# Optimization experiments

Hardware: AMD Instinct MI355X
Metric: run time of the kernel (lower is better)

The kernel has to match this reference:

```python
import jax, jax.numpy as jnp
import numpy as np

HIDDEN = 4096
N_HEADS = 32
N_KV_HEADS = 8
HEAD_DIM = HIDDEN // N_HEADS  # 128
GROUPS = N_HEADS // N_KV_HEADS  # 4
ATTN_MULT = 0.08838834764831845  # 1/sqrt(head_dim)
MAX_ATTN_VAL = 30.0
NEG_INF = -1e30


def setup_inputs() -> dict:
    key = jax.random.key(0)
    ks = jax.random.split(key, 5)
    B, S = 2, 2048
    hidden_states = jax.random.normal(ks[0], (B, S, HIDDEN), dtype=jnp.float32)
    scale = 1.0 / np.sqrt(HIDDEN)
    Wq = jax.random.normal(ks[1], (HIDDEN, N_HEADS * HEAD_DIM), dtype=jnp.float32) * scale
    Wk = jax.random.normal(ks[2], (HIDDEN, N_KV_HEADS * HEAD_DIM), dtype=jnp.float32) * scale
    Wv = jax.random.normal(ks[3], (HIDDEN, N_KV_HEADS * HEAD_DIM), dtype=jnp.float32) * scale
    Wo = jax.random.normal(ks[4], (N_HEADS * HEAD_DIM, HIDDEN), dtype=jnp.float32) * scale
    return {"hidden_states": hidden_states, "Wq": Wq, "Wk": Wk, "Wv": Wv, "Wo": Wo}


def reference(hidden_states, Wq, Wk, Wv, Wo):
    B, S, _ = hidden_states.shape
    # projections
    q = (hidden_states @ Wq).reshape(B, S, N_HEADS, HEAD_DIM).transpose(0, 2, 1, 3)      # bhsd
    k = (hidden_states @ Wk).reshape(B, S, N_KV_HEADS, HEAD_DIM).transpose(0, 2, 1, 3)   # bksd
    v = (hidden_states @ Wv).reshape(B, S, N_KV_HEADS, HEAD_DIM).transpose(0, 2, 1, 3)
    # GQA: expand kv heads to query heads
    k = jnp.repeat(k, GROUPS, axis=1)  # [B, N_HEADS, S, D]
    v = jnp.repeat(v, GROUPS, axis=1)
    # scaled scores with Grok-style tanh soft-cap
    scores = jnp.einsum('bhqd,bhkd->bhqk', q, k) * ATTN_MULT
    scores = MAX_ATTN_VAL * jnp.tanh(scores / MAX_ATTN_VAL)
    # causal mask
    causal = jnp.tril(jnp.ones((S, S), dtype=bool))
    scores = jnp.where(causal[None, None], scores, NEG_INF)
    probs = jax.nn.softmax(scores.astype(jnp.float32), axis=-1).astype(v.dtype)
    out = jnp.einsum('bhqk,bhkd->bhqd', probs, v)          # [B, H, S, D]
    out = out.transpose(0, 2, 1, 3).reshape(B, S, N_HEADS * HEAD_DIM)
    return out @ Wo
```

## Files before the change

kernel.cpp:

```cpp
#include <hip/hip_runtime.h>
#include <hip/hip_bf16.h>
#include <type_traits>
#include <utility>
#include <cmath>

#define HIDDEN 4096
#define NHEADS 32
#define NKV 8
#define HD 128
#define BB 2
#define SS 2048
#define NTOK (BB*SS)
#define ATTN_MULT 0.08838834764831845f

using bf16x8 = __attribute__((ext_vector_type(8))) short;
using f32x4  = __attribute__((ext_vector_type(4))) float;

using gas = __attribute__((address_space(1))) const void;
using las = __attribute__((address_space(3))) void;

__device__ __forceinline__ unsigned short f2bf(float f){
  unsigned int u = __builtin_bit_cast(unsigned int, f);
  u += 0x7fffu + ((u >> 16) & 1u);
  return (unsigned short)(u >> 16);
}
__device__ __forceinline__ unsigned int cvtpk(float lo, float hi){
  unsigned int r;
  asm("v_cvt_pk_bf16_f32 %0, %1, %2" : "=v"(r) : "v"(lo), "v"(hi));
  return r;
}
__device__ __forceinline__ float exp2_hw(float x){
  float r;
  asm("v_exp_f32 %0, %1" : "=v"(r) : "v"(x));
  return r;
}

#define LOG2E 1.4426950408889634f
#define C1L  (-5.3433149e-4f)
#define C2L  (2.3748069e-7f)
#define B30L (-43.280851227f)

__global__ void cvt_f32_bf16_k(const float* __restrict__ in, unsigned short* __restrict__ out, int n8){
  int i = blockIdx.x * blockDim.x + threadIdx.x;
  if (i >= n8) return;
  const float4* p = (const float4*)in + (size_t)i * 2;
  float4 a = p[0], b = p[1];
  bf16x8 o;
  o[0]=f2bf(a.x); o[1]=f2bf(a.y); o[2]=f2bf(a.z); o[3]=f2bf(a.w);
  o[4]=f2bf(b.x); o[5]=f2bf(b.y); o[6]=f2bf(b.z); o[7]=f2bf(b.w);
  ((bf16x8*)out)[i] = o;
}

__global__ void transpose_cvt_k(const float* __restrict__ W, unsigned short* __restrict__ WT, int K, int N){
  __shared__ float tile[32][33];
  int n0 = blockIdx.x * 32, k0 = blockIdx.y * 32;
  int tx = threadIdx.x, ty = threadIdx.y;
  #pragma unroll
  for (int i = 0; i < 4; ++i)
    tile[ty*4+i][tx] = W[(size_t)(k0 + ty*4 + i) * N + n0 + tx];
  __syncthreads();
  #pragma unroll
  for (int i = 0; i < 4; ++i)
    WT[(size_t)(n0 + ty*4 + i) * K + k0 + tx] = f2bf(tile[tx][ty*4+i]);
}

__global__ void transpose_v_k(const unsigned short* __restrict__ in, unsigned short* __restrict__ out){
  __shared__ unsigned short tile[32][33];
  int c0 = blockIdx.x * 32, r0 = blockIdx.y * 32;
  int tx = threadIdx.x, ty = threadIdx.y;
  #pragma unroll
  for (int i = 0; i < 4; ++i)
    tile[ty*4+i][tx] = in[(size_t)(r0 + ty*4 + i) * 2048 + 1024 + c0 + tx];
  __syncthreads();
  #pragma unroll
  for (int i = 0; i < 4; ++i){
    int c = c0 + ty*4 + i, r = r0 + tx;
    out[((size_t)((r >> 11) * 1024 + c)) * 2048 + (r & 2047)] = tile[tx][ty*4+i];
  }
}

template<typename OutT>
__global__ __launch_bounds__(256, 3)
void gemm_bt_k(const unsigned short* __restrict__ A,
               const unsigned short* __restrict__ BT,
               OutT* __restrict__ C, int M, int N, int K){
  __shared__ __align__(16) unsigned short As[128*32];
  __shared__ __align__(16) unsigned short Bs[128*32];
  const int m0 = blockIdx.y * 128, n0 = blockIdx.x * 128;
  const int tid = threadIdx.x, w = tid >> 6, lane = tid & 63;
  const int wr = w >> 1, wc = w & 1;
  const int lrow = lane & 15, lk = (lane >> 4) * 8;
  const int arow = lane >> 2, acol = (lane & 3) * 8;

  f32x4 acc[4][4] = {};

  for (int k0 = 0; k0 < K; k0 += 32){
    #pragma unroll
    for (int i = 0; i < 2; ++i){
      int chunk = w*2 + i;
      const unsigned short* ga = A  + (size_t)(m0 + chunk*16 + arow) * K + k0 + acol;
      const unsigned short* gb = BT + (size_t)(n0 + chunk*16 + arow) * K + k0 + acol;
      __builtin_amdgcn_global_load_lds((gas*)ga, (las*)(As + chunk*512), 16, 0, 0);
      __builtin_amdgcn_global_load_lds((gas*)gb, (las*)(Bs + chunk*512), 16, 0, 0);
    }
    __syncthreads();
    bf16x8 af[4], bfr[4];
    #pragma unroll
    for (int m = 0; m < 4; ++m) af[m]  = *(const bf16x8*)&As[(wr*64 + m*16 + lrow)*32 + lk];
    #pragma unroll
    for (int n = 0; n < 4; ++n) bfr[n] = *(const bf16x8*)&Bs[(wc*64 + n*16 + lrow)*32 + lk];
    #pragma unroll
    for (int m = 0; m < 4; ++m)
      #pragma unroll
      for (int n = 0; n < 4; ++n)
        acc[m][n] = __builtin_amdgcn_mfma_f32_16x16x32_bf16(af[m], bfr[n], acc[m][n], 0, 0, 0);
    __syncthreads();
  }

  const int crow = (lane >> 4) * 4, ccol = lane & 15;
  #pragma unroll
  for (int m = 0; m < 4; ++m)
    #pragma unroll
    for (int n = 0; n < 4; ++n){
      size_t base = (size_t)(m0 + wr*64 + m*16 + crow) * N + n0 + wc*64 + n*16 + ccol;
      #pragma unroll
      for (int r = 0; r < 4; ++r){
        float v = acc[m][n][r];
        if constexpr (std::is_same<OutT, unsigned short>::value) C[base + (size_t)r*N] = f2bf(v);
        else                                                     C[base + (size_t)r*N] = v;
      }
    }
}

#define GBAR() asm volatile("s_barrier" ::: "memory")

#define GEMM_PHASE(P, VMN, STAGE_STMT)                                          \
  {                                                                             \
    bf16x8 af[2][2];                                                            \
    _Pragma("unroll") for (int mi = 0; mi < 2; ++mi)                            \
    _Pragma("unroll") for (int kk = 0; kk < 2; ++kk){                           \
      int row = wm*128 + (P)*32 + mi*16 + lrow;                                 \
      int c8 = (kk*4 + lhi) ^ (row & 7);                                        \
      af[mi][kk] = *(const bf16x8*)&As[cur][row*64 + c8*8];                     \
    }                                                                           \
    if ((P) == 0){                                                              \
      _Pragma("unroll") for (int nf = 0; nf < 4; ++nf)                          \
      _Pragma("unroll") for (int kk = 0; kk < 2; ++kk){                         \
        int row = wn*64 + nf*16 + lrow;                                         \
        int c8 = (kk*4 + lhi) ^ (row & 7);                                      \
        bf[nf][kk] = *(const bf16x8*)&Bs[cur][row*64 + c8*8];                   \
      }                                                                         \
    }                                                                           \
    STAGE_STMT;                                                                 \
    asm volatile("s_waitcnt vmcnt(" #VMN ")");                                  \
    GBAR();                                                                     \
    __builtin_amdgcn_s_setprio(1);                                              \
    _Pragma("unroll") for (int mi = 0; mi < 2; ++mi)                            \
    _Pragma("unroll") for (int nf = 0; nf < 4; ++nf)                            \
    _Pragma("unroll") for (int kk = 0; kk < 2; ++kk)                            \
      acc[(P)*2+mi][nf] = __builtin_amdgcn_mfma_f32_16x16x32_bf16(              \
          af[mi][kk], bf[nf][kk], acc[(P)*2+mi][nf], 0, 0, 0);                  \
    __builtin_amdgcn_s_setprio(0);                                              \
    GBAR();                                                                     \
  }

template<typename OutT>
__global__ __launch_bounds__(512, 2)
void gemm8_k(const unsigned short* __restrict__ A,
             const unsigned short* __restrict__ BT,
             OutT* __restrict__ C, int M, int N, int K, float scale){
  __shared__ __align__(16) unsigned short As[2][256*64];
  __shared__ __align__(16) unsigned short Bs[2][256*64];

  const int nbx = N >> 8;
  const int id = blockIdx.x + blockIdx.y * nbx;
  const int nwg = nbx * (M >> 8);
  const int swz = (id & 7) * (nwg >> 3) + (id >> 3);
  const int m0 = (swz / nbx) << 8, n0 = (swz % nbx) << 8;

  const int tid = threadIdx.x, w = tid >> 6, lane = tid & 63;
  const int wm = w >> 2, wn = w & 3;
  const int lrow = lane & 15, lhi = lane >> 4;
  const int l3 = lane >> 3, k8l = lane & 7;
  const int NT = K >> 6;

  f32x4 acc[8][4] = {};
  bf16x8 bf[4][2];

  auto stageB = [&](int t, int s, int half){
    #pragma unroll
    for (int j = 0; j < 2; ++j){
      int row0 = half*128 + j*64 + w*8;
      int row = row0 + l3;
      const unsigned short* g = BT + (size_t)(n0 + row) * K + t*64 + ((k8l ^ (row & 7)) << 3);
      __builtin_amdgcn_global_load_lds((gas*)g, (las*)(&Bs[s][0] + row0*64), 16, 0, 0);
    }
  };
  auto stageA = [&](int t, int s, int g2){
    #pragma unroll
    for (int j = 0; j < 2; ++j){
      int g = g2 + j;
      int row0 = ((w >= 4) ? 128 : 0) + g*32 + (w & 3)*8;
      int row = row0 + l3;
      const unsigned short* ga = A + (size_t)(m0 + row) * K + t*64 + ((k8l ^ (row & 7)) << 3);
      __builtin_amdgcn_global_load_lds((gas*)ga, (las*)(&As[s][0] + row0*64), 16, 0, 0);
    }
  };

  stageB(0, 0, 0); stageB(0, 0, 1); stageA(0, 0, 0); stageA(0, 0, 2);
  asm volatile("s_waitcnt vmcnt(3)");
  GBAR();

  for (int t = 0; t < NT - 1; ++t){
    const int cur = t & 1, nxt = cur ^ 1;
    GEMM_PHASE(0, 4, stageB(t+1, nxt, 0));
    GEMM_PHASE(1, 5, stageB(t+1, nxt, 1));
    GEMM_PHASE(2, 6, stageA(t+1, nxt, 0));
    GEMM_PHASE(3, 3, stageA(t+1, nxt, 2));
  }
  {
    const int cur = (NT - 1) & 1;
    GEMM_PHASE(0, 2, (void)0);
    GEMM_PHASE(1, 1, (void)0);
    GEMM_PHASE(2, 0, (void)0);
    GEMM_PHASE(3, 0, (void)0);
  }

  #pragma unroll
  for (int mf = 0; mf < 8; ++mf)
    #pragma unroll
    for (int nf = 0; nf < 4; ++nf){
      size_t base = (size_t)(m0 + wm*128 + mf*16 + lhi*4) * N + n0 + wn*64 + nf*16 + lrow;
      #pragma unroll
      for (int r = 0; r < 4; ++r){
        float v = acc[mf][nf][r] * scale;
        if constexpr (std::is_same<OutT, unsigned short>::value) C[base + (size_t)r*N] = f2bf(v);
        else                                                     C[base + (size_t)r*N] = v;
      }
    }
}

__global__ __launch_bounds__(512, 2)
void attn_k(const unsigned short* __restrict__ Q,
            const unsigned short* __restrict__ KVp,
            const unsigned short* __restrict__ VTp,
            unsigned short* __restrict__ ctx){
  __shared__ __align__(16) unsigned short Ks[2][64*128];
  __shared__ __align__(16) unsigned short Vt[2][128*64];
  __shared__ __align__(16) unsigned short Ps[8][1024];

  const int Wb = blockIdx.x;
  const int xcd = Wb & 7, sI = Wb >> 3;
  const int gsub = sI >> 5;
  const int inner = sI & 31;
  const int hsH = inner >> 3;
  const int fi = inner & 7;
  const int group = xcd*2 + gsub;
  const int b = group >> 3, kvh = group & 7;
  const int h = kvh*4 + hsH;

  const int tid = threadIdx.x, w = tid >> 6, lane = tid & 63;
  const int nt = 32 - 2*fi;
  const int lrow = lane & 15, lhi = lane >> 4;
  const int strip = (w < 4) ? fi : (15 - fi);
  const int qwb = strip*128 + (w & 3)*32;
  const int xorv = (lrow & 3) << 4;

  bf16x8 qf[2][4];
  {
    const unsigned short* qb = Q + (size_t)(b*SS + qwb + lrow) * 4096 + h*HD + lhi*8;
    #pragma unroll
    for (int qg = 0; qg < 2; ++qg)
      #pragma unroll
      for (int ks = 0; ks < 4; ++ks)
        qf[qg][ks] = *(const bf16x8*)(qb + (size_t)qg*16*4096 + ks*32);
  }

  f32x4 o[8][2] = {};
  float psum[2] = {0.f, 0.f};

  const unsigned short* Kbh  = KVp + (size_t)b * SS * 2048 + kvh * HD;
  const unsigned short* VTbh = VTp + ((size_t)b * 1024 + kvh * HD) * SS;

  auto STAGE = [&](int db, int t){
    #pragma unroll
    for (int it = 0; it < 2; ++it){
      int cbase = it*512 + w*64;
      int c = cbase + lane;
      int kkv = c >> 4, kc = c & 15;
      const unsigned short* gk = Kbh + (size_t)(t*64 + kkv) * 2048 + ((kc ^ (kkv & 7)) << 3);
      __builtin_amdgcn_global_load_lds((gas*)gk, (las*)(&Ks[db][0] + cbase*8), 16, 0, 0);
      int vd = c >> 3, vc = c & 7;
      const unsigned short* gv = VTbh + (size_t)vd * SS + t*64 + ((vc ^ ((vd ^ (vd >> 3)) & 7)) << 3);
      __builtin_amdgcn_global_load_lds((gas*)gv, (las*)(&Vt[db][0] + cbase*8), 16, 0, 0);
    }
  };

  STAGE(0, 0);
  __syncthreads();

  for (int t = 0; t < nt; ++t){
    const int db = t & 1;
    if (t + 1 < nt) STAGE(db ^ 1, t + 1);

    if (t*64 <= qwb + 31){
      const char* Kc = (const char*)&Ks[db][0];
      const char* Vc = (const char*)&Vt[db][0];
      char* Pw = (char*)&Ps[w][0];

      auto body = [&](auto DIAG){
        #pragma unroll
        for (int hh = 0; hh < 2; ++hh){
          f32x4 sacc[2][2];
          #pragma unroll
          for (int cc = 0; cc < 2; ++cc){
            const int row = (hh*2 + cc)*16 + lrow;
            bf16x8 kf[4];
            #pragma unroll
            for (int ks = 0; ks < 4; ++ks){
              int kbyte = (row*256 + (ks*32 + lhi*8)*2) ^ ((row & 7) << 4);
              kf[ks] = *(const bf16x8*)(Kc + kbyte);
            }
            f32x4 s0 = {0.f,0.f,0.f,0.f}, s1 = {0.f,0.f,0.f,0.f};
            __builtin_amdgcn_s_setprio(1);
            #pragma unroll
            for (int ks = 0; ks < 4; ++ks){
              s0 = __builtin_amdgcn_mfma_f32_16x16x32_bf16(kf[ks], qf[0][ks], s0, 0, 0, 0);
              s1 = __builtin_amdgcn_mfma_f32_16x16x32_bf16(kf[ks], qf[1][ks], s1, 0, 0, 0);
            }
            __builtin_amdgcn_s_setprio(0);
            sacc[0][cc] = s0; sacc[1][cc] = s1;
          }

          #pragma unroll
          for (int qg = 0; qg < 2; ++qg){
            const int qglob = qwb + qg*16 + lrow;
            #pragma unroll
            for (int cc = 0; cc < 2; ++cc){
              float pv[4];
              #pragma unroll
              for (int r = 0; r < 4; ++r){
                float s = __builtin_amdgcn_fmed3f(sacc[qg][cc][r], -25.f, 25.f);
                float s2 = s*s, s4 = s2*s2;
                float wv = __builtin_fmaf(s2, C1L, LOG2E);
                wv = __builtin_fmaf(s4, C2L, wv);
                float p = exp2_hw(__builtin_fmaf(s, wv, B30L));
                if constexpr (decltype(DIAG)::value){
                  int kvg = t*64 + (hh*2 + cc)*16 + lhi*4 + r;
                  p = (kvg <= qglob) ? p : 0.f;
                }
                psum[qg] += p;
                pv[r] = p;
              }
              uint2 pk;
              pk.x = cvtpk(pv[0], pv[1]);
              pk.y = cvtpk(pv[2], pv[3]);
              *(uint2*)(Pw + qg*1024 + lrow*64 + ((cc*32 + lhi*8) ^ xorv)) = pk;
            }
          }

          bf16x8 pf0 = *(const bf16x8*)(Pw +        lrow*64 + ((lhi*16) ^ xorv));
          bf16x8 pf1 = *(const bf16x8*)(Pw + 1024 + lrow*64 + ((lhi*16) ^ xorv));
          __builtin_amdgcn_s_setprio(1);
          #pragma unroll
          for (int df = 0; df < 8; ++df){
            int d = df*16 + lrow;
            int vbyte = (d*128 + (hh*32 + lhi*8)*2) ^ (((d ^ (d >> 3)) & 7) << 4);
            bf16x8 vf = *(const bf16x8*)(Vc + vbyte);
            o[df][0] = __builtin_amdgcn_mfma_f32_16x16x32_bf16(vf, pf0, o[df][0], 0, 0, 0);
            o[df][1] = __builtin_amdgcn_mfma_f32_16x16x32_bf16(vf, pf1, o[df][1], 0, 0, 0);
          }
          __builtin_amdgcn_s_setprio(0);
        }
      };
      if (t == (qwb >> 6)) body(std::true_type{});
      else                 body(std::false_type{});
    }
    __syncthreads();
  }

  #pragma unroll
  for (int qg = 0; qg < 2; ++qg){
    float sum = psum[qg];
    sum += __shfl_xor(sum, 16);
    sum += __shfl_xor(sum, 32);
    float inv = 1.f / sum;
    unsigned short* base = ctx + (size_t)(b*SS + qwb + qg*16 + lrow) * 4096 + h*HD + lhi*4;
    #pragma unroll
    for (int df = 0; df < 8; ++df){
      uint2 pk;
      pk.x = cvtpk(o[df][qg][0] * inv, o[df][qg][1] * inv);
      pk.y = cvtpk(o[df][qg][2] * inv, o[df][qg][3] * inv);
      *(uint2*)(base + df*16) = pk;
    }
  }
}

#define O_HSB   ((size_t)0)
#define O_WQT   ((size_t)33554432)
#define O_WKT   ((size_t)67108864)
#define O_WVT   ((size_t)75497472)
#define O_WOT   ((size_t)83886080)
#define O_Q     ((size_t)117440512)
#define O_KV    ((size_t)150994944)
#define O_CTX   ((size_t)167772160)
#define WS_NEED ((size_t)201326592)

extern "C" void kernel_launch(void* const* d_in, const int* in_sizes, int n_in,
                              void* d_out, int out_size, void* d_ws, size_t ws_size,
                              hipStream_t stream){
  if (ws_size < WS_NEED) return;
  const float* hs = (const float*)d_in[0];
  const float* Wq = (const float*)d_in[1];
  const float* Wk = (const float*)d_in[2];
  const float* Wv = (const float*)d_in[3];
  const float* Wo = (const float*)d_in[4];
  char* ws = (char*)d_ws;
  unsigned short* hsb = (unsigned short*)(ws + O_HSB);
  unsigned short* WqT = (unsigned short*)(ws + O_WQT);
  unsigned short* WkT = (unsigned short*)(ws + O_WKT);
  unsigned short* WvT = (unsigned short*)(ws + O_WVT);
  unsigned short* WoT = (unsigned short*)(ws + O_WOT);
  unsigned short* Qb  = (unsigned short*)(ws + O_Q);
  unsigned short* KVb = (unsigned short*)(ws + O_KV);
  unsigned short* ctxb= (unsigned short*)(ws + O_CTX);
  unsigned short* VTb = (unsigned short*)(ws + O_WQT);

  cvt_f32_bf16_k<<<dim3((NTOK*HIDDEN/8)/256), dim3(256), 0, stream>>>(hs, hsb, NTOK*HIDDEN/8);
  transpose_cvt_k<<<dim3(128,128), dim3(32,8), 0, stream>>>(Wq, WqT, 4096, 4096);
  transpose_cvt_k<<<dim3(32,128),  dim3(32,8), 0, stream>>>(Wk, WkT, 4096, 1024);
  transpose_cvt_k<<<dim3(32,128),  dim3(32,8), 0, stream>>>(Wv, WvT, 4096, 1024);
  transpose_cvt_k<<<dim3(128,128), dim3(32,8), 0, stream>>>(Wo, WoT, 4096, 4096);
  gemm8_k<unsigned short><<<dim3(16,16), dim3(512), 0, stream>>>(hsb, WqT, Qb, 4096, 4096, 4096, ATTN_MULT);
  gemm_bt_k<unsigned short><<<dim3(16,32), dim3(256), 0, stream>>>(hsb, WkT, KVb, 4096, 2048, 4096);
  transpose_v_k<<<dim3(32,128), dim3(32,8), 0, stream>>>(KVb, VTb);
  attn_k<<<dim3(512), dim3(512), 0, stream>>>(Qb, KVb, VTb, ctxb);
  gemm8_k<float><<<dim3(16,16), dim3(512), 0, stream>>>(ctxb, WoT, (float*)d_out, 4096, 4096, 4096, 1.0f);
}
```

Before: 553.9 us.

## Double query rows per wave in attention to reuse K/V fragments

Each wave in the attention kernel now handles 64 query rows (four 16-row groups) instead of 32. Every K and V fragment read from LDS therefore feeds twice as many MFMAs, and the grid halves to 256 blocks. The causal tile count and strip pairing are rescaled to match, and the per-wave P scratch buffer in shared memory is doubled. The cost is many more live registers (Q fragments, output accumulators and row sums), which risks spilling under the existing launch bounds, plus less parallelism across blocks.

```diff
diff --git a/kernel.cpp b/kernel.cpp
--- a/kernel.cpp
+++ b/kernel.cpp
@@ -247,37 +247,37 @@
             unsigned short* __restrict__ ctx){
   __shared__ __align__(16) unsigned short Ks[2][64*128];
   __shared__ __align__(16) unsigned short Vt[2][128*64];
-  __shared__ __align__(16) unsigned short Ps[8][1024];
+  __shared__ __align__(16) unsigned short Ps[8][2048];
 
   const int Wb = blockIdx.x;
   const int xcd = Wb & 7, sI = Wb >> 3;
-  const int gsub = sI >> 5;
-  const int inner = sI & 31;
-  const int hsH = inner >> 3;
-  const int fi = inner & 7;
+  const int gsub = sI >> 4;
+  const int inner = sI & 15;
+  const int hsH = inner >> 2;
+  const int fi = inner & 3;
   const int group = xcd*2 + gsub;
   const int b = group >> 3, kvh = group & 7;
   const int h = kvh*4 + hsH;
 
   const int tid = threadIdx.x, w = tid >> 6, lane = tid & 63;
-  const int nt = 32 - 2*fi;
+  const int nt = (8 - fi) * 4;
   const int lrow = lane & 15, lhi = lane >> 4;
-  const int strip = (w < 4) ? fi : (15 - fi);
-  const int qwb = strip*128 + (w & 3)*32;
+  const int strip = (w < 4) ? fi : (7 - fi);
+  const int qwb = strip*256 + (w & 3)*64;
   const int xorv = (lrow & 3) << 4;
 
-  bf16x8 qf[2][4];
+  bf16x8 qf[4][4];
   {
     const unsigned short* qb = Q + (size_t)(b*SS + qwb + lrow) * 4096 + h*HD + lhi*8;
     #pragma unroll
-    for (int qg = 0; qg < 2; ++qg)
+    for (int qg = 0; qg < 4; ++qg)
       #pragma unroll
       for (int ks = 0; ks < 4; ++ks)
         qf[qg][ks] = *(const bf16x8*)(qb + (size_t)qg*16*4096 + ks*32);
   }
 
-  f32x4 o[8][2] = {};
-  float psum[2] = {0.f, 0.f};
+  f32x4 o[8][4] = {};
+  float psum[4] = {0.f, 0.f, 0.f, 0.f};
 
   const unsigned short* Kbh  = KVp + (size_t)b * SS * 2048 + kvh * HD;
   const unsigned short* VTbh = VTp + ((size_t)b * 1024 + kvh * HD) * SS;
@@ -303,7 +303,7 @@
     const int db = t & 1;
     if (t + 1 < nt) STAGE(db ^ 1, t + 1);
 
-    if (t*64 <= qwb + 31){
+    if (t <= (qwb >> 6)){
       const char* Kc = (const char*)&Ks[db][0];
       const char* Vc = (const char*)&Vt[db][0];
       char* Pw = (char*)&Ps[w][0];
@@ -311,7 +311,6 @@
       auto body = [&](auto DIAG){
         #pragma unroll
         for (int hh = 0; hh < 2; ++hh){
-          f32x4 sacc[2][2];
           #pragma unroll
           for (int cc = 0; cc < 2; ++cc){
             const int row = (hh*2 + cc)*16 + lrow;
@@ -321,26 +320,22 @@
               int kbyte = (row*256 + (ks*32 + lhi*8)*2) ^ ((row & 7) << 4);
               kf[ks] = *(const bf16x8*)(Kc + kbyte);
             }
-            f32x4 s0 = {0.f,0.f,0.f,0.f}, s1 = {0.f,0.f,0.f,0.f};
+            f32x4 sacc[4] = {};
             __builtin_amdgcn_s_setprio(1);
             #pragma unroll
-            for (int ks = 0; ks < 4; ++ks){
-              s0 = __builtin_amdgcn_mfma_f32_16x16x32_bf16(kf[ks], qf[0][ks], s0, 0, 0, 0);
-              s1 = __builtin_amdgcn_mfma_f32_16x16x32_bf16(kf[ks], qf[1][ks], s1, 0, 0, 0);
-            }
+            for (int ks = 0; ks < 4; ++ks)
+              #pragma unroll
+              for (int qg = 0; qg < 4; ++qg)
+                sacc[qg] = __builtin_amdgcn_mfma_f32_16x16x32_bf16(kf[ks], qf[qg][ks], sacc[qg], 0, 0, 0);
             __builtin_amdgcn_s_setprio(0);
-            sacc[0][cc] = s0; sacc[1][cc] = s1;
-          }
-
-          #pragma unroll
-          for (int qg = 0; qg < 2; ++qg){
-            const int qglob = qwb + qg*16 + lrow;
+
             #pragma unroll
-            for (int cc = 0; cc < 2; ++cc){
+            for (int qg = 0; qg < 4; ++qg){
+              const int qglob = qwb + qg*16 + lrow;
               float pv[4];
               #pragma unroll
               for (int r = 0; r < 4; ++r){
-                float s = __builtin_amdgcn_fmed3f(sacc[qg][cc][r], -25.f, 25.f);
+                float s = __builtin_amdgcn_fmed3f(sacc[qg][r], -25.f, 25.f);
                 float s2 = s*s, s4 = s2*s2;
                 float wv = __builtin_fmaf(s2, C1L, LOG2E);
                 wv = __builtin_fmaf(s4, C2L, wv);
@@ -358,17 +353,19 @@
               *(uint2*)(Pw + qg*1024 + lrow*64 + ((cc*32 + lhi*8) ^ xorv)) = pk;
             }
           }
-
-          bf16x8 pf0 = *(const bf16x8*)(Pw +        lrow*64 + ((lhi*16) ^ xorv));
-          bf16x8 pf1 = *(const bf16x8*)(Pw + 1024 + lrow*64 + ((lhi*16) ^ xorv));
+          bf16x8 pf[4];
+          #pragma unroll
+          for (int qg = 0; qg < 4; ++qg)
+            pf[qg] = *(const bf16x8*)(Pw + qg*1024 + lrow*64 + ((lhi*16) ^ xorv));
           __builtin_amdgcn_s_setprio(1);
           #pragma unroll
           for (int df = 0; df < 8; ++df){
             int d = df*16 + lrow;
             int vbyte = (d*128 + (hh*32 + lhi*8)*2) ^ (((d ^ (d >> 3)) & 7) << 4);
             bf16x8 vf = *(const bf16x8*)(Vc + vbyte);
-            o[df][0] = __builtin_amdgcn_mfma_f32_16x16x32_bf16(vf, pf0, o[df][0], 0, 0, 0);
-            o[df][1] = __builtin_amdgcn_mfma_f32_16x16x32_bf16(vf, pf1, o[df][1], 0, 0, 0);
+            #pragma unroll
+            for (int qg = 0; qg < 4; ++qg)
+              o[df][qg] = __builtin_amdgcn_mfma_f32_16x16x32_bf16(vf, pf[qg], o[df][qg], 0, 0, 0);
           }
           __builtin_amdgcn_s_setprio(0);
         }
@@ -380,7 +377,7 @@
   }
 
   #pragma unroll
-  for (int qg = 0; qg < 2; ++qg){
+  for (int qg = 0; qg < 4; ++qg){
     float sum = psum[qg];
     sum += __shfl_xor(sum, 16);
     sum += __shfl_xor(sum, 32);
@@ -434,6 +431,6 @@
   gemm8_k<unsigned short><<<dim3(16,16), dim3(512), 0, stream>>>(hsb, WqT, Qb, 4096, 4096, 4096, ATTN_MULT);
   gemm_bt_k<unsigned short><<<dim3(16,32), dim3(256), 0, stream>>>(hsb, WkT, KVb, 4096, 2048, 4096);
   transpose_v_k<<<dim3(32,128), dim3(32,8), 0, stream>>>(KVb, VTb);
-  attn_k<<<dim3(512), dim3(512), 0, stream>>>(Qb, KVb, VTb, ctxb);
+  attn_k<<<dim3(256), dim3(512), 0, stream>>>(Qb, KVb, VTb, ctxb);
   gemm8_k<float><<<dim3(16,16), dim3(512), 0, stream>>>(ctxb, WoT, (float*)d_out, 4096, 4096, 4096, 1.0f);
 }
```

Measured after the change: 831.6 us. 50.1% more time.
